# Kernel tuning notes

Hardware: AMD Instinct MI355X
Metric: run time of the kernel (lower is better)

Reference implementation:

```python
import jax, jax.numpy as jnp
import numpy as np

WS = 7          # window size
NH = 12         # num heads
DIM = 384       # channels
B, H, W = 16, 56, 56
N = WS * WS     # 49 tokens per window
HD = DIM // NH  # head dim = 32
SCALE = HD ** (-0.5)


def _rel_pos_index():
    # matches the numpy construction in Window_MSA.__init__
    coords = np.stack(np.meshgrid(np.arange(WS), np.arange(WS), indexing='ij'))
    flat = coords.reshape(2, -1)                      # [2, 49]
    rel = flat[:, :, None] - flat[:, None, :]         # [2, 49, 49]
    rel = rel.transpose(1, 2, 0)                      # [49, 49, 2]
    rel[:, :, 0] += WS - 1
    rel[:, :, 1] += WS - 1
    rel[:, :, 0] *= 2 * WS - 1
    return rel.sum(-1)                                # [49, 49] int

_REL_IDX = jnp.asarray(_rel_pos_index())


def setup_inputs() -> dict:
    key = jax.random.key(0)
    ks = jax.random.split(key, 4)
    return {
        'x': jax.random.normal(ks[0], (B, H, W, DIM), dtype=jnp.float32),
        'qkv_w': jax.random.normal(ks[1], (DIM, 3 * DIM), dtype=jnp.float32) * 0.02,
        'qkv_b': jnp.zeros((3 * DIM,), dtype=jnp.float32),
        'proj_w': jax.random.normal(ks[2], (DIM, DIM), dtype=jnp.float32) * 0.02,
        'proj_b': jnp.zeros((DIM,), dtype=jnp.float32),
        'rel_table': jax.random.normal(ks[3], ((2 * WS - 1) ** 2, NH), dtype=jnp.float32) * 0.02,
    }


def reference(x, qkv_w, qkv_b, proj_w, proj_b, rel_table):
    b, h, w, c = x.shape
    nwh, nww = h // WS, w // WS
    # window partition -> [B*nW, N, C]
    xw = x.reshape(b, nwh, WS, nww, WS, c).transpose(0, 1, 3, 2, 4, 5)
    xw = xw.reshape(-1, N, c)
    bn = xw.shape[0]
    # qkv projection -> q,k,v each [bn, NH, N, HD]
    qkv = (xw @ qkv_w + qkv_b).reshape(bn, N, 3, NH, HD).transpose(2, 0, 3, 1, 4)
    q, k, v = qkv[0] * SCALE, qkv[1], qkv[2]
    attn = jax.nn.softmax(jnp.einsum('bhnd,bhmd->bhnm', q, k), axis=-1)
    # NOTE: source adds relative position bias AFTER softmax (faithful quirk)
    bias = rel_table[_REL_IDX.reshape(-1)].reshape(N, N, NH).transpose(2, 0, 1)
    attn = attn + bias[None]
    out = jnp.einsum('bhnm,bhmd->bhnd', attn, v)
    out = out.transpose(0, 2, 1, 3).reshape(bn, N, c)
    out = out @ proj_w + proj_b
    # window reverse -> [B, H, W, C]
    out = out.reshape(b, nwh, nww, WS, WS, c).transpose(0, 1, 3, 2, 4, 5)
    return out.reshape(b, h, w, c)
```

## Files before the change

kernel.cpp:

```cpp
#include <hip/hip_runtime.h>
#include <hip/hip_bf16.h>

typedef unsigned short u16;
typedef __attribute__((ext_vector_type(8))) short bf16x8;
typedef __attribute__((ext_vector_type(4))) float f32x4;

#define NH 12
#define SCALE 0.1767766952966369f

#define UNIT 20992
#define WS_R0    ((size_t)0)
#define WS_QKVB  ((size_t)12288 * UNIT)
#define WS_PROJB (WS_QKVB + (size_t)3 * 12 * 49152)
#define WS_NEED  (WS_PROJB + (size_t)12 * 49152)

__device__ __forceinline__ void split2(float x, u16& h, u16& l) {
    __hip_bfloat16 hb = __float2bfloat16(x);
    float hf = __bfloat162float(hb);
    __hip_bfloat16 lb = __float2bfloat16(x - hf);
    h = __bfloat16_as_ushort(hb);
    l = __bfloat16_as_ushort(lb);
}
__device__ __forceinline__ void split8(const float* v, bf16x8& hi, bf16x8& lo) {
    #pragma unroll
    for (int j = 0; j < 8; ++j) {
        u16 h, l; split2(v[j], h, l);
        hi[j] = (short)h; lo[j] = (short)l;
    }
}

__device__ __forceinline__ void gload16(const char* g, char* l) {
    __builtin_amdgcn_global_load_lds(
        (const __attribute__((address_space(1))) unsigned*)g,
        (__attribute__((address_space(3))) unsigned*)l, 16, 0, 0);
}

__device__ __forceinline__ int swz(int row, int g) {
    return row * 128 + (((g ^ (row & 7)) & 7) << 4);
}

__global__ __launch_bounds__(384) void prep_kernel(
    const float* __restrict__ qkv_w, const float* __restrict__ proj_w,
    char* __restrict__ ws)
{
    const int b = blockIdx.x, row = threadIdx.x;
    float w; size_t base;
    int kl;
    if (b < 1152) {
        int s = b / 384, r = b % 384, ck = r / 32; kl = r % 32;
        w = qkv_w[(size_t)(ck * 32 + kl) * 1152 + s * 384 + row];
        base = WS_QKVB + (size_t)(s * 12 + ck) * 49152;
    } else {
        int b1 = b - 1152, ck = b1 / 32; kl = b1 % 32;
        w = proj_w[(size_t)(ck * 32 + kl) * 384 + row];
        base = WS_PROJB + (size_t)ck * 49152;
    }
    u16 h, l; split2(w, h, l);
    int o = ((row >> 4) * 4 + (kl >> 3)) * 256 + (row & 15) * 16 + (kl & 7) * 2;
    *(u16*)(ws + base + o)         = h;
    *(u16*)(ws + base + 24576 + o) = l;
}

__global__ __launch_bounds__(512, 4) void qkv_gemm_kernel(
    const float* __restrict__ x, const char* __restrict__ wsB,
    const float* __restrict__ qkv_b, char* __restrict__ ws)
{
    __shared__ __align__(16) char bt[49152];

    const int bid0 = blockIdx.x;
    const int bid = (bid0 & 7) * 384 + (bid0 >> 3);
    const int nt = bid % 6, s = nt >> 1, lt = nt & 1;
    const int pair = bid / 6;
    const int tid = threadIdx.x, lane = tid & 63;
    const int wv = tid >> 6;
    const int wm = wv >> 1, wn = wv & 1;
    const int ln = lane & 15, kq = lane >> 4;

    const float* xr[2];
    #pragma unroll
    for (int am = 0; am < 2; ++am) {
        int wwin = pair * 2 + am;
        int bi = wwin >> 6, win = wwin & 63;
        int wy = win >> 3, wx = win & 7;
        int arow = wm * 16 + ln;
        int ar = (arow < 49) ? arow : 0;
        int Y = wy * 7 + ar / 7, X = wx * 7 + ar % 7;
        xr[am] = x + (size_t)((bi * 56 + Y) * 56 + X) * 384 + kq * 8;
    }
    const char* wB = wsB + WS_QKVB + (size_t)s * 12 * 49152;

    auto stage = [&](int ck, int buf) {
        const char* cb = wB + (size_t)ck * 49152 + (size_t)lt * 12288;
        #pragma unroll
        for (int i = 0; i < 3; ++i) {
            int seg = wv + i * 8;
            const char* src = (seg < 12) ? (cb + seg * 1024)
                                         : (cb + 24576 + (seg - 12) * 1024);
            gload16(src + lane * 16, bt + buf * 24576 + seg * 1024);
        }
    };

    stage(0, 0);
    float4 a0A = *(const float4*)(xr[0]);
    float4 a1A = *(const float4*)(xr[0] + 4);
    float4 a0B = *(const float4*)(xr[1]);
    float4 a1B = *(const float4*)(xr[1] + 4);

    f32x4 acc[2][6];
    #pragma unroll
    for (int am = 0; am < 2; ++am)
        #pragma unroll
        for (int f = 0; f < 6; ++f) { acc[am][f][0]=0.f; acc[am][f][1]=0.f; acc[am][f][2]=0.f; acc[am][f][3]=0.f; }

    #pragma unroll 1
    for (int ck = 0; ck < 12; ++ck) {
        const int cur = (ck & 1) * 24576;
        float4 n0A, n1A, n0B, n1B;
        if (ck < 11) {
            stage(ck + 1, (ck & 1) ^ 1);
            n0A = *(const float4*)(xr[0] + (ck + 1) * 32);
            n1A = *(const float4*)(xr[0] + (ck + 1) * 32 + 4);
            n0B = *(const float4*)(xr[1] + (ck + 1) * 32);
            n1B = *(const float4*)(xr[1] + (ck + 1) * 32 + 4);
            asm volatile("s_waitcnt vmcnt(7)" ::: "memory");
        } else {
            asm volatile("s_waitcnt vmcnt(0)" ::: "memory");
        }
        __builtin_amdgcn_s_barrier();
        __builtin_amdgcn_sched_barrier(0);

        bf16x8 ah0, al0, ah1, al1;
        {
            float av[8];
            av[0]=a0A.x; av[1]=a0A.y; av[2]=a0A.z; av[3]=a0A.w;
            av[4]=a1A.x; av[5]=a1A.y; av[6]=a1A.z; av[7]=a1A.w;
            split8(av, ah0, al0);
            av[0]=a0B.x; av[1]=a0B.y; av[2]=a0B.z; av[3]=a0B.w;
            av[4]=a1B.x; av[5]=a1B.y; av[6]=a1B.z; av[7]=a1B.w;
            split8(av, ah1, al1);
        }
        #pragma unroll
        for (int f = 0; f < 6; ++f) {
            int off = cur + ((wn * 6 + f) * 4 + kq) * 256 + ln * 16;
            bf16x8 bh = *(const bf16x8*)(bt + off);
            bf16x8 bl = *(const bf16x8*)(bt + off + 12288);
            acc[0][f] = __builtin_amdgcn_mfma_f32_16x16x32_bf16(ah0, bh, acc[0][f], 0, 0, 0);
            acc[0][f] = __builtin_amdgcn_mfma_f32_16x16x32_bf16(ah0, bl, acc[0][f], 0, 0, 0);
            acc[0][f] = __builtin_amdgcn_mfma_f32_16x16x32_bf16(al0, bh, acc[0][f], 0, 0, 0);
            acc[1][f] = __builtin_amdgcn_mfma_f32_16x16x32_bf16(ah1, bh, acc[1][f], 0, 0, 0);
            acc[1][f] = __builtin_amdgcn_mfma_f32_16x16x32_bf16(ah1, bl, acc[1][f], 0, 0, 0);
            acc[1][f] = __builtin_amdgcn_mfma_f32_16x16x32_bf16(al1, bh, acc[1][f], 0, 0, 0);
        }
        __builtin_amdgcn_sched_barrier(0);
        __builtin_amdgcn_s_barrier();
        if (ck < 11) { a0A = n0A; a1A = n1A; a0B = n0B; a1B = n1B; }
    }

    #pragma unroll
    for (int am = 0; am < 2; ++am) {
        int wwin = pair * 2 + am;
        u16* ub = (u16*)(ws + WS_R0 + (size_t)(wwin * 12) * UNIT);
        #pragma unroll
        for (int f = 0; f < 6; ++f) {
            int n_local = lt * 192 + wn * 96 + f * 16 + ln;
            int hh = n_local >> 5, dd = n_local & 31;
            float bias = qkv_b[s * 384 + n_local];
            u16* u = ub + (size_t)hh * (UNIT / 2);
            #pragma unroll
            for (int r = 0; r < 4; ++r) {
                int wrow = wm * 16 + kq * 4 + r;
                if (wrow < 49) {
                    float val = acc[am][f][r] + bias;
                    if (s == 0) val *= SCALE;
                    u16 h, l; split2(val, h, l);
                    if (s == 0)      { u[wrow * 32 + dd] = h;        u[1568 + wrow * 32 + dd] = l; }
                    else if (s == 1) { u[3136 + wrow * 32 + dd] = h; u[4704 + wrow * 32 + dd] = l; }
                    else             { u[6272 + wrow * 32 + dd] = h; u[8320 + wrow * 32 + dd] = l; }
                }
            }
        }
    }
}

__global__ __launch_bounds__(256) void attn_core_kernel(
    const char* __restrict__ ws, const float* __restrict__ rel_table,
    float* __restrict__ out)
{
    __shared__ __align__(16) float pt[64][68];
    __shared__ __align__(16) float rel_all[2048];
    __shared__ float pmax[4][64];
    __shared__ float psum[4][64];
    __shared__ __align__(16) u16 vth[32][72];
    __shared__ __align__(16) u16 vtl[32][72];

    const int wi = blockIdx.x, bi = wi >> 6, win = wi & 63;
    const int wy = win >> 3, wx = win & 7;
    const int tid = threadIdx.x, lane = tid & 63, wv = tid >> 6;
    const int ln = lane & 15, kq = lane >> 4;

    for (int i = tid; i < 2028; i += 256) rel_all[i] = rel_table[i];
    for (int i = tid; i < 32 * 72; i += 256) { ((u16*)vth)[i] = 0; ((u16*)vtl)[i] = 0; }

    int m7[4], mr[4], outY[4], outX[4];
    bool mok[4];
    #pragma unroll
    for (int r = 0; r < 4; ++r) {
        int m = wv * 16 + kq * 4 + r;
        mok[r] = (m < 49);
        int a = mok[r] ? m : 0;
        m7[r] = a / 7; mr[r] = a % 7;
        outY[r] = wy * 7 + m7[r]; outX[r] = wx * 7 + mr[r];
    }
    int n7[4], nr[4];
    #pragma unroll
    for (int nt = 0; nt < 4; ++nt) {
        int n = nt * 16 + ln, a = (n < 49) ? n : 0;
        n7[nt] = a / 7; nr[nt] = a % 7;
    }
    const int mK = wv * 16 + ln;
    bf16x8 zz;
    #pragma unroll
    for (int j = 0; j < 8; ++j) zz[j] = 0;

    __syncthreads();

    for (int h = 0; h < NH; ++h) {
        const u16* u = (const u16*)(ws + WS_R0 + (size_t)(wi * 12 + h) * UNIT);
        const u16* qhi = u,        * qlo = u + 1568;
        const u16* khi = u + 3136, * klo = u + 4704;
        const u16* vhi = u + 6272, * vlo = u + 8320;

        if (tid < 196) {
            int row = tid >> 2, d0 = (tid & 3) * 8;
            bf16x8 v8h = *(const bf16x8*)(vhi + row * 32 + d0);
            bf16x8 v8l = *(const bf16x8*)(vlo + row * 32 + d0);
            #pragma unroll
            for (int j = 0; j < 8; ++j) {
                vth[d0 + j][row] = (u16)v8h[j];
                vtl[d0 + j][row] = (u16)v8l[j];
            }
        }

        bf16x8 kh = zz, kl = zz;
        if (mK < 49) {
            kh = *(const bf16x8*)(khi + mK * 32 + kq * 8);
            kl = *(const bf16x8*)(klo + mK * 32 + kq * 8);
        }
        f32x4 accs[4];
        #pragma unroll
        for (int nt = 0; nt < 4; ++nt) {
            int n = nt * 16 + ln;
            bf16x8 qh = zz, ql = zz;
            if (n < 49) {
                qh = *(const bf16x8*)(qhi + n * 32 + kq * 8);
                ql = *(const bf16x8*)(qlo + n * 32 + kq * 8);
            }
            f32x4 z; z[0]=0.f; z[1]=0.f; z[2]=0.f; z[3]=0.f;
            z = __builtin_amdgcn_mfma_f32_16x16x32_bf16(kh, qh, z, 0, 0, 0);
            z = __builtin_amdgcn_mfma_f32_16x16x32_bf16(kh, ql, z, 0, 0, 0);
            z = __builtin_amdgcn_mfma_f32_16x16x32_bf16(kl, qh, z, 0, 0, 0);
            accs[nt] = z;
        }

        float e[4][4], gmax[4], ginv[4];
        #pragma unroll
        for (int nt = 0; nt < 4; ++nt) {
            float lm = -3.4e38f;
            #pragma unroll
            for (int r = 0; r < 4; ++r) if (mok[r]) lm = fmaxf(lm, accs[nt][r]);
            lm = fmaxf(lm, __shfl_xor(lm, 16));
            lm = fmaxf(lm, __shfl_xor(lm, 32));
            if (kq == 0) pmax[wv][nt * 16 + ln] = lm;
        }
        __syncthreads();
        #pragma unroll
        for (int nt = 0; nt < 4; ++nt) {
            int n = nt * 16 + ln;
            gmax[nt] = fmaxf(fmaxf(pmax[0][n], pmax[1][n]), fmaxf(pmax[2][n], pmax[3][n]));
            float ls = 0.f;
            #pragma unroll
            for (int r = 0; r < 4; ++r) {
                e[nt][r] = mok[r] ? __expf(accs[nt][r] - gmax[nt]) : 0.f;
                ls += e[nt][r];
            }
            ls += __shfl_xor(ls, 16);
            ls += __shfl_xor(ls, 32);
            if (kq == 0) psum[wv][nt * 16 + ln] = ls;
        }
        __syncthreads();
        #pragma unroll
        for (int nt = 0; nt < 4; ++nt) {
            int n = nt * 16 + ln;
            ginv[nt] = 1.f / (psum[0][n] + psum[1][n] + psum[2][n] + psum[3][n]);
            #pragma unroll
            for (int r = 0; r < 4; ++r) {
                float val = 0.f;
                if (mok[r]) {
                    int bidx = (n7[nt] - m7[r] + 6) * 13 + (nr[nt] - mr[r] + 6);
                    val = e[nt][r] * ginv[nt] + rel_all[bidx * NH + h];
                }
                pt[n][wv * 16 + kq * 4 + r] = val;
            }
        }
        __syncthreads();

        bf16x8 pah[2], pal[2];
        #pragma unroll
        for (int mc = 0; mc < 2; ++mc) {
            const float* pp = &pt[wv * 16 + ln][mc * 32 + kq * 8];
            float v[8];
            float4 a0 = *(const float4*)pp;
            float4 a1 = *(const float4*)(pp + 4);
            v[0]=a0.x; v[1]=a0.y; v[2]=a0.z; v[3]=a0.w;
            v[4]=a1.x; v[5]=a1.y; v[6]=a1.z; v[7]=a1.w;
            split8(v, pah[mc], pal[mc]);
        }
        f32x4 acco[2];
        #pragma unroll
        for (int dt = 0; dt < 2; ++dt) { acco[dt][0]=0.f; acco[dt][1]=0.f; acco[dt][2]=0.f; acco[dt][3]=0.f; }
        #pragma unroll
        for (int dt = 0; dt < 2; ++dt) {
            int d = dt * 16 + ln;
            #pragma unroll
            for (int mc = 0; mc < 2; ++mc) {
                bf16x8 vh = *(const bf16x8*)(&vth[d][mc * 32 + kq * 8]);
                bf16x8 vl = *(const bf16x8*)(&vtl[d][mc * 32 + kq * 8]);
                acco[dt] = __builtin_amdgcn_mfma_f32_16x16x32_bf16(pah[mc], vh, acco[dt], 0, 0, 0);
                acco[dt] = __builtin_amdgcn_mfma_f32_16x16x32_bf16(pah[mc], vl, acco[dt], 0, 0, 0);
                acco[dt] = __builtin_amdgcn_mfma_f32_16x16x32_bf16(pal[mc], vh, acco[dt], 0, 0, 0);
            }
        }
        #pragma unroll
        for (int r = 0; r < 4; ++r) {
            if (mok[r]) {
                size_t base = (size_t)((bi * 56 + outY[r]) * 56 + outX[r]) * 384 + h * 32;
                out[base + ln]      = acco[0][r];
                out[base + 16 + ln] = acco[1][r];
            }
        }
        __syncthreads();
    }
}

__global__ __launch_bounds__(512) void proj_kernel(
    const char* __restrict__ wsB, const float* __restrict__ proj_b,
    float* __restrict__ out)
{
    __shared__ __align__(16) char bt[49152];

    const int tid = threadIdx.x, lane = tid & 63;
    const int wv = tid >> 6, wm = wv >> 1, wn = wv & 1;
    const int ln = lane & 15, kq = lane >> 4;
    const size_t tok0 = (size_t)blockIdx.x * 64;
    const float* xr = out + (tok0 + wm * 16 + ln) * 384 + kq * 8;
    const char* wB = wsB + WS_PROJB;

    bf16x8 st[6];
    #pragma unroll
    for (int i = 0; i < 6; ++i)
        st[i] = *(const bf16x8*)(wB + (size_t)tid * 16 + i * 8192);

    float4 a0 = *(const float4*)(xr);
    float4 a1 = *(const float4*)(xr + 4);

    f32x4 acc[12];
    #pragma unroll
    for (int f = 0; f < 12; ++f) { acc[f][0]=0.f; acc[f][1]=0.f; acc[f][2]=0.f; acc[f][3]=0.f; }

    #pragma unroll 1
    for (int ck = 0; ck < 12; ++ck) {
        __syncthreads();
        #pragma unroll
        for (int i = 0; i < 6; ++i)
            *(bf16x8*)(bt + tid * 16 + i * 8192) = st[i];
        __syncthreads();
        float4 na0, na1;
        if (ck < 11) {
            const char* nb = wB + (size_t)(ck + 1) * 49152;
            #pragma unroll
            for (int i = 0; i < 6; ++i)
                st[i] = *(const bf16x8*)(nb + (size_t)tid * 16 + i * 8192);
            na0 = *(const float4*)(xr + (ck + 1) * 32);
            na1 = *(const float4*)(xr + (ck + 1) * 32 + 4);
        }
        float av[8];
        av[0]=a0.x; av[1]=a0.y; av[2]=a0.z; av[3]=a0.w;
        av[4]=a1.x; av[5]=a1.y; av[6]=a1.z; av[7]=a1.w;
        bf16x8 ah, al; split8(av, ah, al);
        #pragma unroll
        for (int f = 0; f < 12; ++f) {
            int off = (wn * 12 + f) * 1024 + kq * 256 + ln * 16;
            bf16x8 bh = *(const bf16x8*)(bt + off);
            bf16x8 bl = *(const bf16x8*)(bt + 24576 + off);
            acc[f] = __builtin_amdgcn_mfma_f32_16x16x32_bf16(ah, bh, acc[f], 0, 0, 0);
            acc[f] = __builtin_amdgcn_mfma_f32_16x16x32_bf16(ah, bl, acc[f], 0, 0, 0);
            acc[f] = __builtin_amdgcn_mfma_f32_16x16x32_bf16(al, bh, acc[f], 0, 0, 0);
        }
        if (ck < 11) { a0 = na0; a1 = na1; }
    }
    __syncthreads();

    #pragma unroll
    for (int f = 0; f < 12; ++f) {
        int n = wn * 192 + f * 16 + ln;
        float pb = proj_b[n];
        #pragma unroll
        for (int r = 0; r < 4; ++r)
            out[(tok0 + wm * 16 + kq * 4 + r) * 384 + n] = acc[f][r] + pb;
    }
}

__global__ __launch_bounds__(512) void wmsa_attn_kernel(
    const float* __restrict__ x, const float* __restrict__ qkv_w,
    const float* __restrict__ qkv_b, const float* __restrict__ rel_table,
    float* __restrict__ out)
{
    __shared__ __align__(16) char smem[55936];
    u16* bt_hi = (u16*)smem;
    u16* bt_lo = (u16*)(smem + 24576);
    float* qs  = (float*)smem;
    float* kss = (float*)(smem + 14976);
    float* vst = (float*)(smem + 29952);
    float* at  = (float*)(smem + 44288);

    const int wi = blockIdx.x, bi = wi >> 6, win = wi & 63;
    const int wy = win >> 3, wx = win & 7;
    const int tid = threadIdx.x, lane = tid & 63;
    const int wv = tid >> 6, wm = wv >> 1, wn = wv & 1;
    const int ln = lane & 15, kq = lane >> 4;
    const int arow = wm * 16 + ln;

    int Y = wy * 7, X = wx * 7;
    if (arow < 49) { Y += arow / 7; X += arow % 7; }
    const float* xr = x + (size_t)((bi * 56 + Y) * 56 + X) * 384;

    int tcol[3], tkg[3];
    #pragma unroll
    for (int t = 0; t < 3; ++t) { int idx = tid + t * 512; tcol[t] = idx % 192; tkg[t] = idx / 192; }
    float rr[3][8];
    auto loadB = [&](int p, int ck) {
        #pragma unroll
        for (int t = 0; t < 3; ++t) {
            int c = tcol[t];
            int n = (c >> 6) * 384 + p * 64 + (c & 63);
            const float* wp = qkv_w + (size_t)(ck * 64 + tkg[t] * 8) * 1152 + n;
            #pragma unroll
            for (int j = 0; j < 8; ++j) rr[t][j] = wp[(size_t)j * 1152];
        }
    };
    loadB(0, 0);

    #pragma unroll 1
    for (int p = 0; p < 6; ++p) {
        f32x4 acc[6];
        #pragma unroll
        for (int f = 0; f < 6; ++f) { acc[f][0]=0.f; acc[f][1]=0.f; acc[f][2]=0.f; acc[f][3]=0.f; }
        #pragma unroll 1
        for (int ck = 0; ck < 6; ++ck) {
            __syncthreads();
            #pragma unroll
            for (int t = 0; t < 3; ++t) {
                bf16x8 h, l;
                split8(rr[t], h, l);
                *(bf16x8*)((char*)bt_hi + swz(tcol[t], tkg[t])) = h;
                *(bf16x8*)((char*)bt_lo + swz(tcol[t], tkg[t])) = l;
            }
            __syncthreads();
            if (ck < 5) loadB(p, ck + 1);
            else if (p < 5) loadB(p + 1, 0);
            #pragma unroll
            for (int ks = 0; ks < 2; ++ks) {
                float av[8];
                const float* xp = xr + ck * 64 + ks * 32 + kq * 8;
                float4 a0 = *(const float4*)xp;
                float4 a1 = *(const float4*)(xp + 4);
                av[0]=a0.x; av[1]=a0.y; av[2]=a0.z; av[3]=a0.w;
                av[4]=a1.x; av[5]=a1.y; av[6]=a1.z; av[7]=a1.w;
                bf16x8 ah, al; split8(av, ah, al);
                #pragma unroll
                for (int f = 0; f < 6; ++f) {
                    int n = wn * 96 + f * 16 + ln;
                    int off = swz(n, ks * 4 + kq);
                    bf16x8 bh = *(const bf16x8*)((char*)bt_hi + off);
                    bf16x8 bl = *(const bf16x8*)((char*)bt_lo + off);
                    acc[f] = __builtin_amdgcn_mfma_f32_16x16x32_bf16(ah, bh, acc[f], 0, 0, 0);
                    acc[f] = __builtin_amdgcn_mfma_f32_16x16x32_bf16(ah, bl, acc[f], 0, 0, 0);
                    acc[f] = __builtin_amdgcn_mfma_f32_16x16x32_bf16(al, bh, acc[f], 0, 0, 0);
                }
            }
        }
        __syncthreads();
        #pragma unroll
        for (int f = 0; f < 6; ++f) {
            int c = wn * 96 + f * 16 + ln;
            int m = c >> 6, d = c & 63, hh = d >> 5, dd = d & 31;
            float bias = qkv_b[m * 384 + p * 64 + d];
            #pragma unroll
            for (int r = 0; r < 4; ++r) {
                int row = wm * 16 + kq * 4 + r;
                if (row < 52) {
                    float val = acc[f][r] + bias;
                    if (m == 0)      qs [(hh * 52 + row) * 36 + dd] = val * SCALE;
                    else if (m == 1) kss[(hh * 52 + row) * 36 + dd] = val;
                    else             vst[(hh * 32 + dd) * 56 + row] = val;
                }
            }
        }
        __syncthreads();
        for (int hh = 0; hh < 2; ++hh) {
            const int h = p * 2 + hh;
            const float* qsh = qs  + hh * 52 * 36;
            const float* ksh = kss + hh * 52 * 36;
            const float* vsh = vst + hh * 32 * 56;
            if (tid < 169) {
                const int n0 = (tid / 13) * 4, m0 = (tid % 13) * 4;
                float s[4][4] = {};
                #pragma unroll
                for (int k = 0; k < 32; k += 4) {
                    float4 qa[4], kb[4];
                    #pragma unroll
                    for (int i = 0; i < 4; ++i) qa[i] = *(const float4*)&qsh[(n0 + i) * 36 + k];
                    #pragma unroll
                    for (int j = 0; j < 4; ++j) kb[j] = *(const float4*)&ksh[(m0 + j) * 36 + k];
                    #pragma unroll
                    for (int i = 0; i < 4; ++i)
                        #pragma unroll
                        for (int j = 0; j < 4; ++j)
                            s[i][j] += qa[i].x * kb[j].x + qa[i].y * kb[j].y +
                                       qa[i].z * kb[j].z + qa[i].w * kb[j].w;
                }
                #pragma unroll
                for (int i = 0; i < 4; ++i)
                    #pragma unroll
                    for (int j = 0; j < 4; ++j)
                        at[(n0 + i) * 56 + m0 + j] = s[i][j];
            }
            __syncthreads();
            for (int r = wv; r < 49; r += 8) {
                float v = (lane < 49) ? at[r * 56 + lane] : -3.4e38f;
                float mx = v;
                #pragma unroll
                for (int off = 32; off; off >>= 1) mx = fmaxf(mx, __shfl_xor(mx, off));
                float ex = (lane < 49) ? __expf(v - mx) : 0.f;
                float ssum = ex;
                #pragma unroll
                for (int off = 32; off; off >>= 1) ssum += __shfl_xor(ssum, off);
                if (lane < 52) {
                    float res = 0.f;
                    if (lane < 49) {
                        int py = r / 7, px = r % 7, qy = lane / 7, qx = lane % 7;
                        int bidx = (py - qy + 6) * 13 + (px - qx + 6);
                        res = ex / ssum + rel_table[bidx * NH + h];
                    }
                    at[r * 56 + lane] = res;
                }
            }
            __syncthreads();
            if (tid < 208) {
                const int n0 = (tid / 16) * 4, d0 = (tid % 16) * 2;
                float o[4][2] = {};
                #pragma unroll
                for (int m2 = 0; m2 < 52; m2 += 4) {
                    float4 pa[4], vb2[2];
                    #pragma unroll
                    for (int i = 0; i < 4; ++i) pa[i] = *(const float4*)&at[(n0 + i) * 56 + m2];
                    #pragma unroll
                    for (int j = 0; j < 2; ++j) vb2[j] = *(const float4*)&vsh[(d0 + j) * 56 + m2];
                    #pragma unroll
                    for (int i = 0; i < 4; ++i)
                        #pragma unroll
                        for (int j = 0; j < 2; ++j)
                            o[i][j] += pa[i].x * vb2[j].x + pa[i].y * vb2[j].y +
                                       pa[i].z * vb2[j].z + pa[i].w * vb2[j].w;
                }
                #pragma unroll
                for (int i = 0; i < 4; ++i) {
                    int n = n0 + i;
                    if (n < 49) {
                        int Yo = wy * 7 + n / 7, Xo = wx * 7 + n % 7;
                        size_t base = (size_t)((bi * 56 + Yo) * 56 + Xo) * 384 + h * 32 + d0;
                        *(float2*)(out + base) = make_float2(o[i][0], o[i][1]);
                    }
                }
            }
            __syncthreads();
        }
    }
}

__global__ __launch_bounds__(512) void wmsa_proj_kernel(
    const float* __restrict__ proj_w, const float* __restrict__ proj_b,
    float* __restrict__ out)
{
    __shared__ __align__(16) char smem[98304];
    u16* bt_hi = (u16*)smem;
    u16* bt_lo = (u16*)(smem + 49152);

    const int tid = threadIdx.x, lane = tid & 63;
    const int wv = tid >> 6, wm = wv >> 1, wn = wv & 1;
    const int ln = lane & 15, kq = lane >> 4;
    const size_t tok0 = (size_t)blockIdx.x * 64;
    const float* xr = out + (tok0 + wm * 16 + ln) * 384;

    int tcol[6], tkg[6];
    #pragma unroll
    for (int t = 0; t < 6; ++t) { int idx = tid + t * 512; tcol[t] = idx % 384; tkg[t] = idx / 384; }
    float rr[6][8];
    auto loadB = [&](int ck) {
        #pragma unroll
        for (int t = 0; t < 6; ++t) {
            const float* wp = proj_w + (size_t)(ck * 64 + tkg[t] * 8) * 384 + tcol[t];
            #pragma unroll
            for (int j = 0; j < 8; ++j) rr[t][j] = wp[(size_t)j * 384];
        }
    };
    loadB(0);

    f32x4 acc[12];
    #pragma unroll
    for (int f = 0; f < 12; ++f) { acc[f][0]=0.f; acc[f][1]=0.f; acc[f][2]=0.f; acc[f][3]=0.f; }

    #pragma unroll 1
    for (int ck = 0; ck < 6; ++ck) {
        __syncthreads();
        #pragma unroll
        for (int t = 0; t < 6; ++t) {
            bf16x8 h, l; split8(rr[t], h, l);
            *(bf16x8*)((char*)bt_hi + swz(tcol[t], tkg[t])) = h;
            *(bf16x8*)((char*)bt_lo + swz(tcol[t], tkg[t])) = l;
        }
        __syncthreads();
        if (ck < 5) loadB(ck + 1);
        #pragma unroll
        for (int ks = 0; ks < 2; ++ks) {
            float av[8];
            const float* xp = xr + ck * 64 + ks * 32 + kq * 8;
            float4 a0 = *(const float4*)xp;
            float4 a1 = *(const float4*)(xp + 4);
            av[0]=a0.x; av[1]=a0.y; av[2]=a0.z; av[3]=a0.w;
            av[4]=a1.x; av[5]=a1.y; av[6]=a1.z; av[7]=a1.w;
            bf16x8 ah, al; split8(av, ah, al);
            #pragma unroll
            for (int f = 0; f < 12; ++f) {
                int n = wn * 192 + f * 16 + ln;
                int off = swz(n, ks * 4 + kq);
                bf16x8 bh = *(const bf16x8*)((char*)bt_hi + off);
                bf16x8 bl = *(const bf16x8*)((char*)bt_lo + off);
                acc[f] = __builtin_amdgcn_mfma_f32_16x16x32_bf16(ah, bh, acc[f], 0, 0, 0);
                acc[f] = __builtin_amdgcn_mfma_f32_16x16x32_bf16(ah, bl, acc[f], 0, 0, 0);
                acc[f] = __builtin_amdgcn_mfma_f32_16x16x32_bf16(al, bh, acc[f], 0, 0, 0);
            }
        }
    }
    __syncthreads();

    #pragma unroll
    for (int f = 0; f < 12; ++f) {
        int n = wn * 192 + f * 16 + ln;
        float pb = proj_b[n];
        #pragma unroll
        for (int r = 0; r < 4; ++r)
            out[(tok0 + wm * 16 + kq * 4 + r) * 384 + n] = acc[f][r] + pb;
    }
}

extern "C" void kernel_launch(void* const* d_in, const int* in_sizes, int n_in,
                              void* d_out, int out_size, void* d_ws, size_t ws_size,
                              hipStream_t stream) {
    const float* x         = (const float*)d_in[0];
    const float* qkv_w     = (const float*)d_in[1];
    const float* qkv_b     = (const float*)d_in[2];
    const float* proj_w    = (const float*)d_in[3];
    const float* proj_b    = (const float*)d_in[4];
    const float* rel_table = (const float*)d_in[5];
    float* out = (float*)d_out;
    char* wsc = (char*)d_ws;

    if (ws_size >= WS_NEED) {
        hipLaunchKernelGGL(prep_kernel, dim3(1536), dim3(384), 0, stream,
                           qkv_w, proj_w, wsc);
        hipLaunchKernelGGL(qkv_gemm_kernel, dim3(3072), dim3(512), 0, stream,
                           x, wsc, qkv_b, wsc);
        hipLaunchKernelGGL(attn_core_kernel, dim3(1024), dim3(256), 0, stream,
                           wsc, rel_table, out);
        hipLaunchKernelGGL(proj_kernel, dim3(784), dim3(512), 0, stream,
                           wsc, proj_b, out);
    } else {
        hipLaunchKernelGGL(wmsa_attn_kernel, dim3(1024), dim3(512), 0, stream,
                           x, qkv_w, qkv_b, rel_table, out);
        hipLaunchKernelGGL(wmsa_proj_kernel, dim3(784), dim3(512), 0, stream,
                           proj_w, proj_b, out);
    }
}
```

Measured before the change: 421.7 us.

## Halve QKV GEMM block to 4 waves with two row groups per wave

The QKV GEMM block shrinks from 512 to 256 threads, so each wave now covers two 16-row groups per window and reuses each B fragment read from LDS across four MFMA tiles instead of two. The register prefetch of the next A chunk is removed: A loads for the current chunk are issued at the top of each iteration alongside staging of the next B chunk, with the wait count adjusted. This cuts LDS reads per MFMA and barrier participants, at the cost of more accumulator registers (lower occupancy target of 3) and exposing A load latency within each iteration.

```diff
diff --git a/kernel.cpp b/kernel.cpp
--- a/kernel.cpp
+++ b/kernel.cpp
@@ -61,7 +61,7 @@
     *(u16*)(ws + base + 24576 + o) = l;
 }
 
-__global__ __launch_bounds__(512, 4) void qkv_gemm_kernel(
+__global__ __launch_bounds__(256, 3) void qkv_gemm_kernel(
     const float* __restrict__ x, const char* __restrict__ wsB,
     const float* __restrict__ qkv_b, char* __restrict__ ws)
 {
@@ -76,24 +76,27 @@
     const int wm = wv >> 1, wn = wv & 1;
     const int ln = lane & 15, kq = lane >> 4;
 
-    const float* xr[2];
+    const float* xr[2][2];
     #pragma unroll
     for (int am = 0; am < 2; ++am) {
         int wwin = pair * 2 + am;
         int bi = wwin >> 6, win = wwin & 63;
         int wy = win >> 3, wx = win & 7;
-        int arow = wm * 16 + ln;
-        int ar = (arow < 49) ? arow : 0;
-        int Y = wy * 7 + ar / 7, X = wx * 7 + ar % 7;
-        xr[am] = x + (size_t)((bi * 56 + Y) * 56 + X) * 384 + kq * 8;
+        #pragma unroll
+        for (int rg = 0; rg < 2; ++rg) {
+            int arow = (wm * 2 + rg) * 16 + ln;
+            int ar = (arow < 49) ? arow : 0;
+            int Y = wy * 7 + ar / 7, X = wx * 7 + ar % 7;
+            xr[am][rg] = x + (size_t)((bi * 56 + Y) * 56 + X) * 384 + kq * 8;
+        }
     }
     const char* wB = wsB + WS_QKVB + (size_t)s * 12 * 49152;
 
     auto stage = [&](int ck, int buf) {
         const char* cb = wB + (size_t)ck * 49152 + (size_t)lt * 12288;
         #pragma unroll
-        for (int i = 0; i < 3; ++i) {
-            int seg = wv + i * 8;
+        for (int i = 0; i < 6; ++i) {
+            int seg = wv + i * 4;
             const char* src = (seg < 12) ? (cb + seg * 1024)
                                          : (cb + 24576 + (seg - 12) * 1024);
             gload16(src + lane * 16, bt + buf * 24576 + seg * 1024);
@@ -101,59 +104,61 @@
     };
 
     stage(0, 0);
-    float4 a0A = *(const float4*)(xr[0]);
-    float4 a1A = *(const float4*)(xr[0] + 4);
-    float4 a0B = *(const float4*)(xr[1]);
-    float4 a1B = *(const float4*)(xr[1] + 4);
-
-    f32x4 acc[2][6];
+
+    f32x4 acc[2][2][6];
     #pragma unroll
     for (int am = 0; am < 2; ++am)
         #pragma unroll
-        for (int f = 0; f < 6; ++f) { acc[am][f][0]=0.f; acc[am][f][1]=0.f; acc[am][f][2]=0.f; acc[am][f][3]=0.f; }
+        for (int rg = 0; rg < 2; ++rg)
+            #pragma unroll
+            for (int f = 0; f < 6; ++f) { acc[am][rg][f][0]=0.f; acc[am][rg][f][1]=0.f; acc[am][rg][f][2]=0.f; acc[am][rg][f][3]=0.f; }
 
     #pragma unroll 1
     for (int ck = 0; ck < 12; ++ck) {
         const int cur = (ck & 1) * 24576;
-        float4 n0A, n1A, n0B, n1B;
+        float4 ar[2][2][2];
+        #pragma unroll
+        for (int am = 0; am < 2; ++am)
+            #pragma unroll
+            for (int rg = 0; rg < 2; ++rg) {
+                ar[am][rg][0] = *(const float4*)(xr[am][rg] + ck * 32);
+                ar[am][rg][1] = *(const float4*)(xr[am][rg] + ck * 32 + 4);
+            }
         if (ck < 11) {
             stage(ck + 1, (ck & 1) ^ 1);
-            n0A = *(const float4*)(xr[0] + (ck + 1) * 32);
-            n1A = *(const float4*)(xr[0] + (ck + 1) * 32 + 4);
-            n0B = *(const float4*)(xr[1] + (ck + 1) * 32);
-            n1B = *(const float4*)(xr[1] + (ck + 1) * 32 + 4);
-            asm volatile("s_waitcnt vmcnt(7)" ::: "memory");
+            asm volatile("s_waitcnt vmcnt(6)" ::: "memory");
         } else {
             asm volatile("s_waitcnt vmcnt(0)" ::: "memory");
         }
         __builtin_amdgcn_s_barrier();
         __builtin_amdgcn_sched_barrier(0);
 
-        bf16x8 ah0, al0, ah1, al1;
-        {
-            float av[8];
-            av[0]=a0A.x; av[1]=a0A.y; av[2]=a0A.z; av[3]=a0A.w;
-            av[4]=a1A.x; av[5]=a1A.y; av[6]=a1A.z; av[7]=a1A.w;
-            split8(av, ah0, al0);
-            av[0]=a0B.x; av[1]=a0B.y; av[2]=a0B.z; av[3]=a0B.w;
-            av[4]=a1B.x; av[5]=a1B.y; av[6]=a1B.z; av[7]=a1B.w;
-            split8(av, ah1, al1);
-        }
+        bf16x8 ah[2][2], al[2][2];
+        #pragma unroll
+        for (int am = 0; am < 2; ++am)
+            #pragma unroll
+            for (int rg = 0; rg < 2; ++rg) {
+                float av[8];
+                av[0]=ar[am][rg][0].x; av[1]=ar[am][rg][0].y; av[2]=ar[am][rg][0].z; av[3]=ar[am][rg][0].w;
+                av[4]=ar[am][rg][1].x; av[5]=ar[am][rg][1].y; av[6]=ar[am][rg][1].z; av[7]=ar[am][rg][1].w;
+                split8(av, ah[am][rg], al[am][rg]);
+            }
         #pragma unroll
         for (int f = 0; f < 6; ++f) {
             int off = cur + ((wn * 6 + f) * 4 + kq) * 256 + ln * 16;
             bf16x8 bh = *(const bf16x8*)(bt + off);
             bf16x8 bl = *(const bf16x8*)(bt + off + 12288);
-            acc[0][f] = __builtin_amdgcn_mfma_f32_16x16x32_bf16(ah0, bh, acc[0][f], 0, 0, 0);
-            acc[0][f] = __builtin_amdgcn_mfma_f32_16x16x32_bf16(ah0, bl, acc[0][f], 0, 0, 0);
-            acc[0][f] = __builtin_amdgcn_mfma_f32_16x16x32_bf16(al0, bh, acc[0][f], 0, 0, 0);
-            acc[1][f] = __builtin_amdgcn_mfma_f32_16x16x32_bf16(ah1, bh, acc[1][f], 0, 0, 0);
-            acc[1][f] = __builtin_amdgcn_mfma_f32_16x16x32_bf16(ah1, bl, acc[1][f], 0, 0, 0);
-            acc[1][f] = __builtin_amdgcn_mfma_f32_16x16x32_bf16(al1, bh, acc[1][f], 0, 0, 0);
+            #pragma unroll
+            for (int am = 0; am < 2; ++am)
+                #pragma unroll
+                for (int rg = 0; rg < 2; ++rg) {
+                    acc[am][rg][f] = __builtin_amdgcn_mfma_f32_16x16x32_bf16(ah[am][rg], bh, acc[am][rg][f], 0, 0, 0);
+                    acc[am][rg][f] = __builtin_amdgcn_mfma_f32_16x16x32_bf16(ah[am][rg], bl, acc[am][rg][f], 0, 0, 0);
+                    acc[am][rg][f] = __builtin_amdgcn_mfma_f32_16x16x32_bf16(al[am][rg], bh, acc[am][rg][f], 0, 0, 0);
+                }
         }
         __builtin_amdgcn_sched_barrier(0);
         __builtin_amdgcn_s_barrier();
-        if (ck < 11) { a0A = n0A; a1A = n1A; a0B = n0B; a1B = n1B; }
     }
 
     #pragma unroll
@@ -167,15 +172,18 @@
             float bias = qkv_b[s * 384 + n_local];
             u16* u = ub + (size_t)hh * (UNIT / 2);
             #pragma unroll
-            for (int r = 0; r < 4; ++r) {
-                int wrow = wm * 16 + kq * 4 + r;
-                if (wrow < 49) {
-                    float val = acc[am][f][r] + bias;
-                    if (s == 0) val *= SCALE;
-                    u16 h, l; split2(val, h, l);
-                    if (s == 0)      { u[wrow * 32 + dd] = h;        u[1568 + wrow * 32 + dd] = l; }
-                    else if (s == 1) { u[3136 + wrow * 32 + dd] = h; u[4704 + wrow * 32 + dd] = l; }
-                    else             { u[6272 + wrow * 32 + dd] = h; u[8320 + wrow * 32 + dd] = l; }
+            for (int rg = 0; rg < 2; ++rg) {
+                #pragma unroll
+                for (int r = 0; r < 4; ++r) {
+                    int wrow = (wm * 2 + rg) * 16 + kq * 4 + r;
+                    if (wrow < 49) {
+                        float val = acc[am][rg][f][r] + bias;
+                        if (s == 0) val *= SCALE;
+                        u16 h, l; split2(val, h, l);
+                        if (s == 0)      { u[wrow * 32 + dd] = h;        u[1568 + wrow * 32 + dd] = l; }
+                        else if (s == 1) { u[3136 + wrow * 32 + dd] = h; u[4704 + wrow * 32 + dd] = l; }
+                        else             { u[6272 + wrow * 32 + dd] = h; u[8320 + wrow * 32 + dd] = l; }
+                    }
                 }
             }
         }
@@ -679,7 +687,7 @@
     if (ws_size >= WS_NEED) {
         hipLaunchKernelGGL(prep_kernel, dim3(1536), dim3(384), 0, stream,
                            qkv_w, proj_w, wsc);
-        hipLaunchKernelGGL(qkv_gemm_kernel, dim3(3072), dim3(512), 0, stream,
+        hipLaunchKernelGGL(qkv_gemm_kernel, dim3(3072), dim3(256), 0, stream,
                            x, wsc, qkv_b, wsc);
         hipLaunchKernelGGL(attn_core_kernel, dim3(1024), dim3(256), 0, stream,
                            wsc, rel_table, out);
```

Result: slower. 439.4 us (+4.2%).
